# Kernel tuning notes

Hardware: AMD Instinct MI355X
Metric: run time of the kernel (lower is better)

Reference implementation:

```python
import jax, jax.numpy as jnp
import numpy as np

D = 2048
EPS = 1e-5


def setup_inputs() -> dict:
    key = jax.random.key(0)
    ks = jax.random.split(key, 6)
    B, T = 4, 4096
    gain = 2 ** (-2.5)
    scale = gain * np.sqrt(6.0 / (D + D))  # xavier_uniform bound
    def w(k):
        return jax.random.uniform(k, (D, D), jnp.float32, -scale, scale)
    return {
        "hidden_states": jax.random.normal(ks[0], (B, T, D), jnp.float32),
        "Wi": w(ks[1]),  # i_proj.weight^T laid out as [in, out]
        "Wf": w(ks[2]),
        "Wg": w(ks[3]),
        "Wo": w(ks[4]),
        "g_norm_weight": jnp.ones((D,), jnp.float32),
    }


def _hgrn_scan(a, b):
    # solves h_t = a_t * h_{t-1} + b_t elementwise, parallel over time axis 1
    def comb(c1, c2):
        a1, b1 = c1
        a2, b2 = c2
        return (a1 * a2, b1 * a2 + b2)
    _, h = jax.lax.associative_scan(comb, (a, b), axis=1)
    return h


def reference(hidden_states, Wi, Wf, Wg, Wo, g_norm_weight):
    x = hidden_states  # [B, T, D]
    i_raw = jnp.einsum("btd,de->bte", x, Wi)
    f_raw = jnp.einsum("btd,de->bte", x, Wf)
    # swiglu(i, 1 - sigmoid(f)) = silu(i) * (1 - sigmoid(f)); f = logsigmoid(f)
    i = jax.nn.silu(i_raw) * jax.nn.sigmoid(-f_raw)  # 1 - sigmoid(f) = sigmoid(-f)
    a = jnp.exp(jax.nn.log_sigmoid(f_raw))  # forget gate in (0, 1)
    o = _hgrn_scan(a, i)  # [B, T, D] linear recurrence output
    # FusedRMSNormSwishGate: RMSNorm(o) * weight, gated by g * sigmoid(g)
    g = jnp.einsum("btd,de->bte", x, Wg)
    rms = o * jax.lax.rsqrt(jnp.mean(o * o, axis=-1, keepdims=True) + EPS)
    o = (rms * g_norm_weight) * (g * jax.nn.sigmoid(g))
    return jnp.einsum("btd,de->bte", o, Wo)
```

## Files before the change

### kernel.cpp

```cpp
#include <hip/hip_runtime.h>
#include <hip/hip_bf16.h>
#include <stdint.h>

#define Dm  2048
#define Tt  4096
#define Bb  4
#define Rr  4096
#define NCH 64
#define TCH 64
#define EPSf 1e-5f

typedef __attribute__((ext_vector_type(8))) short short8;
typedef __attribute__((ext_vector_type(4))) float f32x4;

__device__ __forceinline__ unsigned short f2bf(float x) {
  unsigned u = __builtin_bit_cast(unsigned, x);
  u += 0x7FFFu + ((u >> 16) & 1u);
  return (unsigned short)(u >> 16);
}
__device__ __forceinline__ float bf2f(unsigned short b) {
  unsigned u = ((unsigned)b) << 16;
  return __builtin_bit_cast(float, u);
}
__device__ __forceinline__ float sigmoidf_(float x) {
  return 1.0f / (1.0f + __expf(-x));
}
__device__ __forceinline__ void gload16(const void* g, void* l) {
  __builtin_amdgcn_global_load_lds(
      (const __attribute__((address_space(1))) unsigned int*)g,
      (__attribute__((address_space(3))) unsigned int*)l, 16, 0, 0);
}

__global__ __launch_bounds__(256) void k_sentinel(float* __restrict__ out, int n) {
  int i = blockIdx.x * 256 + threadIdx.x;
  if (i < n) out[i] = 12345.0f;
}

__global__ __launch_bounds__(256) void k_split(const float* __restrict__ in,
                                               short* __restrict__ hi,
                                               short* __restrict__ lo) {
  size_t i = (size_t)blockIdx.x * 256 + threadIdx.x;
  const float4* p = (const float4*)in + i * 2;
  float4 a = p[0], b = p[1];
  float v[8] = {a.x,a.y,a.z,a.w,b.x,b.y,b.z,b.w};
  short8 h, l;
#pragma unroll
  for (int j = 0; j < 8; ++j) {
    unsigned short hb = f2bf(v[j]);
    h[j] = (short)hb;
    l[j] = (short)f2bf(v[j] - bf2f(hb));
  }
  ((short8*)hi)[i] = h;
  ((short8*)lo)[i] = l;
}

__global__ __launch_bounds__(256) void k_convw(const float* __restrict__ W,
                                               short* __restrict__ hi,
                                               short* __restrict__ lo) {
  __shared__ float t[64][65];
  const int n0 = blockIdx.x * 64, k0 = blockIdx.y * 64;
  const int tid = threadIdx.x;
  const int r = tid >> 6, c = tid & 63;
#pragma unroll
  for (int rr = r; rr < 64; rr += 4)
    t[rr][c] = W[(size_t)(k0 + rr) * Dm + n0 + c];
  __syncthreads();
#pragma unroll
  for (int rr = r; rr < 64; rr += 4) {
    float v = t[c][rr];
    unsigned short hb = f2bf(v);
    size_t o = (size_t)(n0 + rr) * Dm + k0 + c;
    hi[o] = (short)hb;
    lo[o] = (short)f2bf(v - bf2f(hb));
  }
}

#define BM 128
#define BN 128
#define BK 32

__global__ __launch_bounds__(256, 2) void k_gemm(
    const short* __restrict__ Ah, const short* __restrict__ Al,
    const short* __restrict__ Bh, const short* __restrict__ Bl,
    float* __restrict__ C, int M, int N, int K) {
  __shared__ __align__(16) short sAh[BM*BK], sAl[BM*BK], sBh[BN*BK], sBl[BN*BK];
  const int tid  = threadIdx.x;
  const int lane = tid & 63;
  const int wave = tid >> 6;
  const int ntn  = N / BN;
  const int bx   = blockIdx.x % ntn;
  const int by   = blockIdx.x / ntn;
  const int m0 = by * BM, n0 = bx * BN;

  const int c0 = tid,        r0 = c0 >> 2, p0 = (c0 & 3) ^ ((r0 >> 1) & 3);
  const int c1 = tid + 256,  r1 = c1 >> 2, p1 = (c1 & 3) ^ ((r1 >> 1) & 3);
  const size_t ga0 = (size_t)(m0 + r0) * K + p0 * 8;
  const size_t ga1 = (size_t)(m0 + r1) * K + p1 * 8;
  const size_t gb0 = (size_t)(n0 + r0) * K + p0 * 8;
  const size_t gb1 = (size_t)(n0 + r1) * K + p1 * 8;

  const int wr = wave >> 1, wc = wave & 1;
  const int l15 = lane & 15, kg = lane >> 4;
  int aoff[4], boff[4];
#pragma unroll
  for (int f = 0; f < 4; ++f) {
    int ar = wr * 64 + f * 16 + l15;
    aoff[f] = ar * BK + (kg ^ ((ar >> 1) & 3)) * 8;
    int br = wc * 64 + f * 16 + l15;
    boff[f] = br * BK + (kg ^ ((br >> 1) & 3)) * 8;
  }

  f32x4 acc[4][4] = {};

  for (int kk = 0; kk < K; kk += BK) {
    gload16(Ah + ga0 + kk, sAh + c0 * 8);
    gload16(Ah + ga1 + kk, sAh + c1 * 8);
    gload16(Al + ga0 + kk, sAl + c0 * 8);
    gload16(Al + ga1 + kk, sAl + c1 * 8);
    gload16(Bh + gb0 + kk, sBh + c0 * 8);
    gload16(Bh + gb1 + kk, sBh + c1 * 8);
    gload16(Bl + gb0 + kk, sBl + c0 * 8);
    gload16(Bl + gb1 + kk, sBl + c1 * 8);
    __syncthreads();

    short8 ah[4], al[4], bh[4], bl[4];
#pragma unroll
    for (int f = 0; f < 4; ++f) {
      ah[f] = *(const short8*)(sAh + aoff[f]);
      al[f] = *(const short8*)(sAl + aoff[f]);
      bh[f] = *(const short8*)(sBh + boff[f]);
      bl[f] = *(const short8*)(sBl + boff[f]);
    }
#pragma unroll
    for (int mf = 0; mf < 4; ++mf)
#pragma unroll
      for (int nf = 0; nf < 4; ++nf)
        acc[mf][nf] = __builtin_amdgcn_mfma_f32_16x16x32_bf16(ah[mf], bh[nf], acc[mf][nf], 0, 0, 0);
#pragma unroll
    for (int mf = 0; mf < 4; ++mf)
#pragma unroll
      for (int nf = 0; nf < 4; ++nf)
        acc[mf][nf] = __builtin_amdgcn_mfma_f32_16x16x32_bf16(al[mf], bh[nf], acc[mf][nf], 0, 0, 0);
#pragma unroll
    for (int mf = 0; mf < 4; ++mf)
#pragma unroll
      for (int nf = 0; nf < 4; ++nf)
        acc[mf][nf] = __builtin_amdgcn_mfma_f32_16x16x32_bf16(ah[mf], bl[nf], acc[mf][nf], 0, 0, 0);
    __syncthreads();
  }

#pragma unroll
  for (int mf = 0; mf < 4; ++mf)
#pragma unroll
    for (int nf = 0; nf < 4; ++nf) {
      const int crow = m0 + wr * 64 + mf * 16 + kg * 4;
      const int ccol = n0 + wc * 64 + nf * 16 + l15;
      float* cp = C + (size_t)crow * N + ccol;
#pragma unroll
      for (int r = 0; r < 4; ++r)
        cp[(size_t)r * N] = acc[mf][nf][r];
    }
}

__global__ __launch_bounds__(256) void k_scan1(float* __restrict__ fP,
                                               float* __restrict__ iH,
                                               float* __restrict__ Ps,
                                               float* __restrict__ Hs) {
  const int c = blockIdx.x;
  const int d = blockIdx.y * 256 + threadIdx.x;
  size_t idx = (size_t)c * TCH * Dm + d;
  float h = 0.f, P = 1.f;
  for (int t = 0; t < TCH; ++t, idx += Dm) {
    float f = fP[idx], iv = iH[idx];
    float a  = sigmoidf_(f);
    float ig = iv * sigmoidf_(iv) * (1.f - a);
    h = __builtin_fmaf(a, h, ig);
    P *= a;
    iH[idx] = h;
    fP[idx] = P;
  }
  size_t s = (size_t)c * Dm + d;
  Ps[s] = P;
  Hs[s] = h;
}

__global__ __launch_bounds__(256) void k_scan2(const float* __restrict__ Ps,
                                               const float* __restrict__ Hs,
                                               float* __restrict__ cy) {
  const int d = blockIdx.x * 256 + threadIdx.x;
  float c = 0.f;
  for (int ch = 0; ch < NCH; ++ch) {
    size_t s = (size_t)ch * Dm + d;
    cy[s] = c;
    c = Hs[s] + Ps[s] * c;
  }
}

__global__ __launch_bounds__(256) void k_scan3(const float* __restrict__ fP,
                                               float* __restrict__ oH,
                                               const float* __restrict__ cyb) {
  const int c = blockIdx.x;
  const int d = blockIdx.y * 256 + threadIdx.x;
  size_t s = (size_t)c * Dm + d;
  float cy = cyb[s];
  if (__all(cy == 0.f)) return;
  size_t idx = (size_t)c * TCH * Dm + d;
  for (int t = 0; t < TCH; ++t, idx += Dm)
    oH[idx] = __builtin_fmaf(fP[idx], cy, oH[idx]);
}

__global__ __launch_bounds__(256) void k_norm(const float* __restrict__ o,
                                              const float* __restrict__ g,
                                              const float* __restrict__ gw,
                                              short* __restrict__ oh,
                                              short* __restrict__ ol) {
  const int row = blockIdx.x;
  const size_t base = (size_t)row * Dm;
  const int tid = threadIdx.x;
  const float4* po = (const float4*)(o + base) + tid * 2;
  float4 o0 = po[0], o1 = po[1];
  float ss = o0.x*o0.x + o0.y*o0.y + o0.z*o0.z + o0.w*o0.w
           + o1.x*o1.x + o1.y*o1.y + o1.z*o1.z + o1.w*o1.w;
#pragma unroll
  for (int off = 32; off > 0; off >>= 1) ss += __shfl_down(ss, off, 64);
  __shared__ float red[4];
  if ((tid & 63) == 0) red[tid >> 6] = ss;
  __syncthreads();
  const float rms = rsqrtf((red[0] + red[1] + red[2] + red[3]) * (1.0f / Dm) + EPSf);
  const float4* pg = (const float4*)(g + base) + tid * 2;
  float4 g0 = pg[0], g1 = pg[1];
  const float4* pw = (const float4*)gw + tid * 2;
  float4 w0 = pw[0], w1 = pw[1];
  float ov[8] = {o0.x,o0.y,o0.z,o0.w,o1.x,o1.y,o1.z,o1.w};
  float gv[8] = {g0.x,g0.y,g0.z,g0.w,g1.x,g1.y,g1.z,g1.w};
  float wv[8] = {w0.x,w0.y,w0.z,w0.w,w1.x,w1.y,w1.z,w1.w};
  short8 h8, l8;
#pragma unroll
  for (int j = 0; j < 8; ++j) {
    float val = ov[j] * rms * wv[j] * (gv[j] * sigmoidf_(gv[j]));
    unsigned short hb = f2bf(val);
    h8[j] = (short)hb;
    l8[j] = (short)f2bf(val - bf2f(hb));
  }
  ((short8*)(oh + base))[tid] = h8;
  ((short8*)(ol + base))[tid] = l8;
}

extern "C" void kernel_launch(void* const* d_in, const int* in_sizes, int n_in,
                              void* d_out, int out_size, void* d_ws, size_t ws_size,
                              hipStream_t stream) {
  const float* x   = (const float*)d_in[0];
  const float* Wi  = (const float*)d_in[1];
  const float* Wf  = (const float*)d_in[2];
  const float* Wg  = (const float*)d_in[3];
  const float* Wo  = (const float*)d_in[4];
  const float* gnw = (const float*)d_in[5];
  float* out = (float*)d_out;
  char* ws = (char*)d_ws;

  const size_t WOFF = 0;
  const size_t XHI  = 67108864ULL;
  const size_t XLO  = 83886080ULL;
  const size_t GI   = 100663296ULL;
  const size_t GF   = 134217728ULL;
  const size_t GG   = 167772160ULL;
  const size_t PS   = 201326592ULL;
  const size_t HS   = 201850880ULL;
  const size_t CY   = 202375168ULL;
  const size_t NEED = 202899456ULL;

  if (ws_size < NEED) {
    k_sentinel<<<(out_size + 255) / 256, 256, 0, stream>>>(out, out_size);
    return;
  }

  short* x_hi = (short*)(ws + XHI);
  short* x_lo = (short*)(ws + XLO);
  float* gi   = (float*)(ws + GI);
  float* gf   = (float*)(ws + GF);
  float* gg   = (float*)(ws + GG);
  float* Psum = (float*)(ws + PS);
  float* Hsum = (float*)(ws + HS);
  float* carry= (float*)(ws + CY);

  short* wbuf = (short*)(ws + WOFF);
  const size_t WSZ = (size_t)Dm * Dm;
  short* Wih = wbuf + 0 * WSZ; short* Wil = wbuf + 1 * WSZ;
  short* Wfh = wbuf + 2 * WSZ; short* Wfl = wbuf + 3 * WSZ;
  short* Wgh = wbuf + 4 * WSZ; short* Wgl = wbuf + 5 * WSZ;
  short* Woh = wbuf + 6 * WSZ; short* Wol = wbuf + 7 * WSZ;

  dim3 gwt(Dm / 64, Dm / 64);
  k_convw<<<gwt, 256, 0, stream>>>(Wi, Wih, Wil);
  k_convw<<<gwt, 256, 0, stream>>>(Wf, Wfh, Wfl);
  k_convw<<<gwt, 256, 0, stream>>>(Wg, Wgh, Wgl);
  k_convw<<<gwt, 256, 0, stream>>>(Wo, Woh, Wol);

  const int gblocks = (Rr / BM) * (Dm / BN);
  const dim3 gsc(NCH, Dm / 256);

  for (int b = 0; b < Bb; ++b) {
    const size_t rowoff = (size_t)b * Rr * Dm;

    k_split<<<(Rr * Dm / 8) / 256, 256, 0, stream>>>(x + rowoff, x_hi, x_lo);

    k_gemm<<<gblocks, 256, 0, stream>>>(x_hi, x_lo, Wih, Wil, gi, Rr, Dm, Dm);
    k_gemm<<<gblocks, 256, 0, stream>>>(x_hi, x_lo, Wfh, Wfl, gf, Rr, Dm, Dm);
    k_gemm<<<gblocks, 256, 0, stream>>>(x_hi, x_lo, Wgh, Wgl, gg, Rr, Dm, Dm);

    k_scan1<<<gsc, 256, 0, stream>>>(gf, gi, Psum, Hsum);
    k_scan2<<<Dm / 256, 256, 0, stream>>>(Psum, Hsum, carry);
    k_scan3<<<gsc, 256, 0, stream>>>(gf, gi, carry);

    k_norm<<<Rr, 256, 0, stream>>>(gi, gg, gnw, x_hi, x_lo);

    k_gemm<<<gblocks, 256, 0, stream>>>(x_hi, x_lo, Woh, Wol, out + rowoff, Rr, Dm, Dm);
  }
}
```

Baseline: 2.080 ms.

## Fuse three input-projection GEMMs into one and batch the output GEMM

The i/f/g projection weights now sit contiguously, so a single GEMM with N=3*D covers all three. Its epilogue remaps columns into three separate [M,D] output planes, which gi, gf and gg already occupy back to back. When the workspace is large enough, the normalized activations for all batches go to a separate buffer and one output GEMM covers all 4*4096 rows. The change also adds a blockIdx swizzle over groups of eight blocks for cache locality and raises the launch-bounds occupancy hint from 2 to 4, which may force register spills.

```diff
diff --git a/kernel.cpp b/kernel.cpp
--- a/kernel.cpp
+++ b/kernel.cpp
@@ -79,7 +79,7 @@
 #define BN 128
 #define BK 32
 
-__global__ __launch_bounds__(256, 2) void k_gemm(
+__global__ __launch_bounds__(256, 4) void k_gemm(
     const short* __restrict__ Ah, const short* __restrict__ Al,
     const short* __restrict__ Bh, const short* __restrict__ Bl,
     float* __restrict__ C, int M, int N, int K) {
@@ -88,8 +88,11 @@
   const int lane = tid & 63;
   const int wave = tid >> 6;
   const int ntn  = N / BN;
-  const int bx   = blockIdx.x % ntn;
-  const int by   = blockIdx.x / ntn;
+  const int nwg = (int)gridDim.x;
+  const int bid = (int)blockIdx.x;
+  const int swz = (bid & 7) * (nwg >> 3) + (bid >> 3);
+  const int bx  = swz % ntn;
+  const int by  = swz / ntn;
   const int m0 = by * BM, n0 = bx * BN;
 
   const int c0 = tid,        r0 = c0 >> 2, p0 = (c0 & 3) ^ ((r0 >> 1) & 3);
@@ -155,10 +158,11 @@
     for (int nf = 0; nf < 4; ++nf) {
       const int crow = m0 + wr * 64 + mf * 16 + kg * 4;
       const int ccol = n0 + wc * 64 + nf * 16 + l15;
-      float* cp = C + (size_t)crow * N + ccol;
+      const int mat = ccol >> 11, cc = ccol & 2047;
+      float* cp = C + ((size_t)mat * M + crow) * 2048 + cc;
 #pragma unroll
       for (int r = 0; r < 4; ++r)
-        cp[(size_t)r * N] = acc[mf][nf][r];
+        cp[(size_t)r * 2048] = acc[mf][nf][r];
     }
 }
 
@@ -268,11 +272,15 @@
   const size_t HS   = 201850880ULL;
   const size_t CY   = 202375168ULL;
   const size_t NEED = 202899456ULL;
+  const size_t O2HI = NEED;
+  const size_t O2LO = NEED + 67108864ULL;
+  const size_t NEED_BIG = NEED + 134217728ULL;
 
   if (ws_size < NEED) {
     k_sentinel<<<(out_size + 255) / 256, 256, 0, stream>>>(out, out_size);
     return;
   }
+  const bool big = (ws_size >= NEED_BIG);
 
   short* x_hi = (short*)(ws + XHI);
   short* x_lo = (short*)(ws + XLO);
@@ -282,21 +290,24 @@
   float* Psum = (float*)(ws + PS);
   float* Hsum = (float*)(ws + HS);
   float* carry= (float*)(ws + CY);
+  short* o2hi = (short*)(ws + O2HI);
+  short* o2lo = (short*)(ws + O2LO);
 
   short* wbuf = (short*)(ws + WOFF);
   const size_t WSZ = (size_t)Dm * Dm;
-  short* Wih = wbuf + 0 * WSZ; short* Wil = wbuf + 1 * WSZ;
-  short* Wfh = wbuf + 2 * WSZ; short* Wfl = wbuf + 3 * WSZ;
-  short* Wgh = wbuf + 4 * WSZ; short* Wgl = wbuf + 5 * WSZ;
-  short* Woh = wbuf + 6 * WSZ; short* Wol = wbuf + 7 * WSZ;
+  short* Whi3 = wbuf;
+  short* Wlo3 = wbuf + 3 * WSZ;
+  short* Woh  = wbuf + 6 * WSZ;
+  short* Wol  = wbuf + 7 * WSZ;
 
   dim3 gwt(Dm / 64, Dm / 64);
-  k_convw<<<gwt, 256, 0, stream>>>(Wi, Wih, Wil);
-  k_convw<<<gwt, 256, 0, stream>>>(Wf, Wfh, Wfl);
-  k_convw<<<gwt, 256, 0, stream>>>(Wg, Wgh, Wgl);
+  k_convw<<<gwt, 256, 0, stream>>>(Wi, Whi3 + 0 * WSZ, Wlo3 + 0 * WSZ);
+  k_convw<<<gwt, 256, 0, stream>>>(Wf, Whi3 + 1 * WSZ, Wlo3 + 1 * WSZ);
+  k_convw<<<gwt, 256, 0, stream>>>(Wg, Whi3 + 2 * WSZ, Wlo3 + 2 * WSZ);
   k_convw<<<gwt, 256, 0, stream>>>(Wo, Woh, Wol);
 
-  const int gblocks = (Rr / BM) * (Dm / BN);
+  const int gfused = (Rr / BM) * (3 * Dm / BN);
+  const int gout1  = (Rr / BM) * (Dm / BN);
   const dim3 gsc(NCH, Dm / 256);
 
   for (int b = 0; b < Bb; ++b) {
@@ -304,16 +315,22 @@
 
     k_split<<<(Rr * Dm / 8) / 256, 256, 0, stream>>>(x + rowoff, x_hi, x_lo);
 
-    k_gemm<<<gblocks, 256, 0, stream>>>(x_hi, x_lo, Wih, Wil, gi, Rr, Dm, Dm);
-    k_gemm<<<gblocks, 256, 0, stream>>>(x_hi, x_lo, Wfh, Wfl, gf, Rr, Dm, Dm);
-    k_gemm<<<gblocks, 256, 0, stream>>>(x_hi, x_lo, Wgh, Wgl, gg, Rr, Dm, Dm);
+    k_gemm<<<gfused, 256, 0, stream>>>(x_hi, x_lo, Whi3, Wlo3, gi, Rr, 3 * Dm, Dm);
 
     k_scan1<<<gsc, 256, 0, stream>>>(gf, gi, Psum, Hsum);
     k_scan2<<<Dm / 256, 256, 0, stream>>>(Psum, Hsum, carry);
     k_scan3<<<gsc, 256, 0, stream>>>(gf, gi, carry);
 
-    k_norm<<<Rr, 256, 0, stream>>>(gi, gg, gnw, x_hi, x_lo);
-
-    k_gemm<<<gblocks, 256, 0, stream>>>(x_hi, x_lo, Woh, Wol, out + rowoff, Rr, Dm, Dm);
-  }
-}
+    if (big) {
+      k_norm<<<Rr, 256, 0, stream>>>(gi, gg, gnw, o2hi + rowoff, o2lo + rowoff);
+    } else {
+      k_norm<<<Rr, 256, 0, stream>>>(gi, gg, gnw, x_hi, x_lo);
+      k_gemm<<<gout1, 256, 0, stream>>>(x_hi, x_lo, Woh, Wol, out + rowoff, Rr, Dm, Dm);
+    }
+  }
+
+  if (big) {
+    const int goutB = (Bb * Rr / BM) * (Dm / BN);
+    k_gemm<<<goutB, 256, 0, stream>>>(o2hi, o2lo, Woh, Wol, out, Bb * Rr, Dm, Dm);
+  }
+}
```

New measurement: 2.232 ms. +7.3%, slower.
